# Kernel optimization log

Hardware: AMD Instinct MI355X
Metric: run time of the kernel (lower is better)

The kernel has to match this reference:

```python
import jax, jax.numpy as jnp
import numpy as np

LN_EPS = 1e-5


def setup_inputs() -> dict:
    N, E, D = 50000, 800000, 128
    H = 4 * D
    key = jax.random.key(0)
    ks = jax.random.split(key, 8)
    h = jax.random.normal(ks[0], (N, D), dtype=jnp.float32)
    e_ij = jax.random.normal(ks[1], (E, D), dtype=jnp.float32)
    src = jax.random.randint(ks[2], (E,), 0, N, dtype=jnp.int32)
    dst = jax.random.randint(ks[3], (E,), 0, N, dtype=jnp.int32)
    # MLP params (torch nn.Linear default-style scale)
    W1 = jax.random.normal(ks[4], (D, H), dtype=jnp.float32) / np.sqrt(D)
    b1 = jnp.zeros((H,), dtype=jnp.float32)
    W2 = jax.random.normal(ks[5], (H, D), dtype=jnp.float32) / np.sqrt(H)
    b2 = jnp.zeros((D,), dtype=jnp.float32)
    gamma = jnp.ones((D,), dtype=jnp.float32)
    beta = jnp.zeros((D,), dtype=jnp.float32)
    return {"h": h, "e_ij": e_ij, "src": src, "dst": dst,
            "W1": W1, "b1": b1, "W2": W2, "b2": b2,
            "gamma": gamma, "beta": beta}


def reference(h, e_ij, src, dst, W1, b1, W2, b2, gamma, beta):
    N = h.shape[0]
    # update_all(copy_u('h'), sum): sum source-node features at each destination
    neigh = jax.ops.segment_sum(h[src], dst, num_segments=N)
    # update_all(copy_edge('e_ij'), sum): sum edge features at each destination
    u_edge = jax.ops.segment_sum(e_ij, dst, num_segments=N)
    u = neigh + u_edge                      # [N, D]
    # MLP: D -> 4D -> D with ReLU, then residual
    hid = jax.nn.relu(u @ W1 + b1)          # [N, 4D]
    out = hid @ W2 + b2 + h                 # [N, D]
    # LayerNorm over feature dim
    mean = jnp.mean(out, axis=-1, keepdims=True)
    var = jnp.var(out, axis=-1, keepdims=True)
    normed = (out - mean) * jax.lax.rsqrt(var + LN_EPS)
    # dropout with training=False is identity
    return normed * gamma + beta
```

## Files before the change

### kernel.cpp

```cpp
#include <hip/hip_runtime.h>

#define BM 64

typedef __bf16 bf16x8 __attribute__((ext_vector_type(8)));
typedef float f32x4 __attribute__((ext_vector_type(4)));
typedef float f4 __attribute__((ext_vector_type(4)));

__device__ __forceinline__ unsigned short f2bf(float x) {
  unsigned int u = __builtin_bit_cast(unsigned int, x);
  u += 0x7fffu + ((u >> 16) & 1u);
  return (unsigned short)(u >> 16);
}

__device__ __forceinline__ int swz(int row, int col) {
  return (row * 128 + col) ^ ((row & 7) << 3);
}

__device__ __forceinline__ f4 ntload4(const float* p) {
  return __builtin_nontemporal_load((const f4*)p);
}

__device__ __forceinline__ int wave_incl_scan(int v, int lane) {
  #pragma unroll
  for (int off = 1; off < 64; off <<= 1) {
    int t = __shfl_up(v, off, 64);
    if (lane >= off) v += t;
  }
  return v;
}

__global__ __launch_bounds__(256) void prep_weights(
    const float* __restrict__ W1, const float* __restrict__ W2,
    unsigned short* __restrict__ W1T, unsigned short* __restrict__ W2T,
    int* __restrict__ counts, int N) {
  int t = blockIdx.x * 256 + threadIdx.x;
  if (t < N) counts[t] = 0;
  {
    int hh = t >> 7, kk = t & 127;
    W1T[t] = f2bf(W1[kk * 512 + hh]);
  }
  {
    int dd = t >> 9, hh = t & 511;
    W2T[t] = f2bf(W2[hh * 128 + dd]);
  }
}

__global__ __launch_bounds__(256) void hist_dst(const int* __restrict__ dst,
                                                int* counts, int E) {
  int i = blockIdx.x * 256 + threadIdx.x;
  if (i < E) atomicAdd(&counts[dst[i]], 1);
}

__global__ __launch_bounds__(256) void scan1(const int* __restrict__ counts,
                                             int* offs, int* btot, int N) {
  int i = blockIdx.x * 256 + threadIdx.x;
  int lane = threadIdx.x & 63, wv = threadIdx.x >> 6;
  int v = (i < N) ? counts[i] : 0;
  int incl = wave_incl_scan(v, lane);
  __shared__ int wt[4];
  if (lane == 63) wt[wv] = incl;
  __syncthreads();
  int wpre = 0;
  for (int w = 0; w < wv; ++w) wpre += wt[w];
  if (i < N) offs[i] = wpre + incl - v;
  if (threadIdx.x == 255) btot[blockIdx.x] = wpre + incl;
}

__global__ __launch_bounds__(64) void scan2(int* btot, int nb) {
  int lane = threadIdx.x;
  __shared__ int carry_s;
  if (lane == 0) carry_s = 0;
  __syncthreads();
  for (int base = 0; base < nb; base += 64) {
    int i = base + lane;
    int v = (i < nb) ? btot[i] : 0;
    int incl = wave_incl_scan(v, lane);
    int carry = carry_s;
    if (i < nb) btot[i] = carry + incl - v;
    __syncthreads();
    if (lane == 63) carry_s = carry + incl;
    __syncthreads();
  }
}

__global__ __launch_bounds__(256) void scan3(int* offs, const int* __restrict__ btot,
                                             int N) {
  int i = blockIdx.x * 256 + threadIdx.x;
  if (i < N) offs[i] += btot[blockIdx.x];
}

__global__ __launch_bounds__(256) void build_perm(const int* __restrict__ dst,
                                                  const int* __restrict__ src,
                                                  int* offs, int2* perm2, int E) {
  int i = blockIdx.x * 256 + threadIdx.x;
  if (i < E) {
    int p = atomicAdd(&offs[dst[i]], 1);
    perm2[p] = make_int2(i, src[i]);
  }
}

__global__ __launch_bounds__(256) void gather_sum(
    const float* __restrict__ hfeat, const float* __restrict__ eij,
    const int2* __restrict__ perm2,
    const int* __restrict__ offs, const int* __restrict__ counts,
    float* __restrict__ u, int N) {
  int node = blockIdx.x * 4 + (threadIdx.x >> 6);
  if (node >= N) return;
  int lane = threadIdx.x & 63;
  int half = lane >> 5, c4 = (lane & 31) * 4;
  int cnt = counts[node];
  int beg = offs[node] - cnt;
  f4 acc = (f4){0.f, 0.f, 0.f, 0.f};
  for (int base = 0; base < cnt; base += 64) {
    int m = cnt - base; if (m > 64) m = 64;
    int2 es = perm2[beg + base + (lane < m ? lane : m - 1)];
    int k = 0;
    for (; 2 * k + 8 <= m; k += 4) {
      int i0 = 2 * k + half;
      int e0 = __shfl(es.x, i0, 64),     s0 = __shfl(es.y, i0, 64);
      int e1 = __shfl(es.x, i0 + 2, 64), s1 = __shfl(es.y, i0 + 2, 64);
      int e2 = __shfl(es.x, i0 + 4, 64), s2 = __shfl(es.y, i0 + 4, 64);
      int e3 = __shfl(es.x, i0 + 6, 64), s3 = __shfl(es.y, i0 + 6, 64);
      f4 ev0 = ntload4(eij + (size_t)e0 * 128 + c4);
      f4 ev1 = ntload4(eij + (size_t)e1 * 128 + c4);
      f4 ev2 = ntload4(eij + (size_t)e2 * 128 + c4);
      f4 ev3 = ntload4(eij + (size_t)e3 * 128 + c4);
      f4 hv0 = *(const f4*)(hfeat + (size_t)s0 * 128 + c4);
      f4 hv1 = *(const f4*)(hfeat + (size_t)s1 * 128 + c4);
      f4 hv2 = *(const f4*)(hfeat + (size_t)s2 * 128 + c4);
      f4 hv3 = *(const f4*)(hfeat + (size_t)s3 * 128 + c4);
      acc += (ev0 + hv0) + (ev1 + hv1) + (ev2 + hv2) + (ev3 + hv3);
    }
    for (; 2 * k < m; ++k) {
      int idx = 2 * k + half;
      int e = __shfl(es.x, idx & 63, 64), s = __shfl(es.y, idx & 63, 64);
      if (idx < m) {
        f4 ev = ntload4(eij + (size_t)e * 128 + c4);
        f4 hv = *(const f4*)(hfeat + (size_t)s * 128 + c4);
        acc += ev + hv;
      }
    }
  }
  acc.x += __shfl_xor(acc.x, 32, 64);
  acc.y += __shfl_xor(acc.y, 32, 64);
  acc.z += __shfl_xor(acc.z, 32, 64);
  acc.w += __shfl_xor(acc.w, 32, 64);
  if (half == 0) *(f4*)(u + (size_t)node * 128 + c4) = acc;
}

__global__ __launch_bounds__(256, 2) void fused_mlp_ln(
    float* uo, const float* __restrict__ hfeat,
    const unsigned short* __restrict__ W1T, const unsigned short* __restrict__ W2T,
    const float* __restrict__ b1, const float* __restrict__ b2,
    const float* __restrict__ gma, const float* __restrict__ bta, int N) {
  __shared__ unsigned short As[BM * 128];
  __shared__ unsigned short Hs[BM * 128];
  __shared__ unsigned short Bs[128 * 128];

  const int tid = threadIdx.x;
  const int wave = tid >> 6, lane = tid & 63;
  const int lo = lane & 15, hi = lane >> 4;
  const int bm0 = blockIdx.x * BM;
  const int arow = wave * 16 + lo;

  #pragma unroll
  for (int i = 0; i < 8; ++i) {
    int q = i * 256 + tid;
    int r = q >> 5, c4 = (q & 31) * 4;
    f4 v = (f4){0.f, 0.f, 0.f, 0.f};
    if (bm0 + r < N) v = *(const f4*)(uo + (size_t)(bm0 + r) * 128 + c4);
    uint2 bv;
    bv.x = (unsigned)f2bf(v.x) | ((unsigned)f2bf(v.y) << 16);
    bv.y = (unsigned)f2bf(v.z) | ((unsigned)f2bf(v.w) << 16);
    *(uint2*)(&As[swz(r, c4)]) = bv;
  }

  f32x4 acc2[8];
  #pragma unroll
  for (int n = 0; n < 8; ++n) acc2[n] = (f32x4){0.f, 0.f, 0.f, 0.f};

  for (int c = 0; c < 4; ++c) {
    __syncthreads();
    #pragma unroll
    for (int i = 0; i < 8; ++i) {
      int q = i * 256 + tid;
      int r = q >> 4, c8 = (q & 15) * 8;
      uint4 w = *(const uint4*)(W1T + ((size_t)(c * 128 + r) * 128 + c8));
      *(uint4*)(&Bs[swz(r, c8)]) = w;
    }
    __syncthreads();

    f32x4 acc1[8];
    #pragma unroll
    for (int n = 0; n < 8; ++n) acc1[n] = (f32x4){0.f, 0.f, 0.f, 0.f};
    #pragma unroll
    for (int kk = 0; kk < 4; ++kk) {
      bf16x8 a = *(const bf16x8*)(&As[swz(arow, kk * 32 + hi * 8)]);
      #pragma unroll
      for (int n = 0; n < 8; ++n) {
        bf16x8 b = *(const bf16x8*)(&Bs[swz(n * 16 + lo, kk * 32 + hi * 8)]);
        acc1[n] = __builtin_amdgcn_mfma_f32_16x16x32_bf16(a, b, acc1[n], 0, 0, 0);
      }
    }
    #pragma unroll
    for (int n = 0; n < 8; ++n) {
      float bb = b1[c * 128 + n * 16 + lo];
      #pragma unroll
      for (int j = 0; j < 4; ++j) {
        float v = acc1[n][j] + bb;
        v = v > 0.f ? v : 0.f;
        Hs[swz(wave * 16 + hi * 4 + j, n * 16 + lo)] = f2bf(v);
      }
    }
    __syncthreads();
    #pragma unroll
    for (int i = 0; i < 8; ++i) {
      int q = i * 256 + tid;
      int r = q >> 4, c8 = (q & 15) * 8;
      uint4 w = *(const uint4*)(W2T + ((size_t)r * 512 + c * 128 + c8));
      *(uint4*)(&Bs[swz(r, c8)]) = w;
    }
    __syncthreads();
    #pragma unroll
    for (int kk = 0; kk < 4; ++kk) {
      bf16x8 a = *(const bf16x8*)(&Hs[swz(arow, kk * 32 + hi * 8)]);
      #pragma unroll
      for (int n = 0; n < 8; ++n) {
        bf16x8 b = *(const bf16x8*)(&Bs[swz(n * 16 + lo, kk * 32 + hi * 8)]);
        acc2[n] = __builtin_amdgcn_mfma_f32_16x16x32_bf16(a, b, acc2[n], 0, 0, 0);
      }
    }
  }

  float b2v[8], gv[8], bv2[8];
  #pragma unroll
  for (int n = 0; n < 8; ++n) {
    int d = n * 16 + lo;
    b2v[n] = b2[d]; gv[n] = gma[d]; bv2[n] = bta[d];
  }
  #pragma unroll
  for (int j = 0; j < 4; ++j) {
    int m = wave * 16 + hi * 4 + j;
    int grow = bm0 + m;
    bool valid = grow < N;
    float vals[8];
    float s = 0.f, s2 = 0.f;
    #pragma unroll
    for (int n = 0; n < 8; ++n) {
      float hres = valid ? hfeat[(size_t)grow * 128 + n * 16 + lo] : 0.f;
      float v = acc2[n][j] + b2v[n] + hres;
      vals[n] = v;
      s += v; s2 += v * v;
    }
    #pragma unroll
    for (int mk = 1; mk < 16; mk <<= 1) {
      s  += __shfl_xor(s, mk, 64);
      s2 += __shfl_xor(s2, mk, 64);
    }
    float mean = s * (1.f / 128.f);
    float var = s2 * (1.f / 128.f) - mean * mean;
    float inv = rsqrtf(var + 1e-5f);
    if (valid) {
      #pragma unroll
      for (int n = 0; n < 8; ++n) {
        uo[(size_t)grow * 128 + n * 16 + lo] = (vals[n] - mean) * inv * gv[n] + bv2[n];
      }
    }
  }
}

extern "C" void kernel_launch(void* const* d_in, const int* in_sizes, int n_in,
                              void* d_out, int out_size, void* d_ws, size_t ws_size,
                              hipStream_t stream) {
  (void)n_in; (void)out_size; (void)ws_size;
  const float* hfeat = (const float*)d_in[0];
  const float* eij   = (const float*)d_in[1];
  const int*   src   = (const int*)d_in[2];
  const int*   dst   = (const int*)d_in[3];
  const float* W1    = (const float*)d_in[4];
  const float* b1    = (const float*)d_in[5];
  const float* W2    = (const float*)d_in[6];
  const float* b2    = (const float*)d_in[7];
  const float* gma   = (const float*)d_in[8];
  const float* bta   = (const float*)d_in[9];
  float* out = (float*)d_out;

  int N = in_sizes[0] / 128;
  int E = in_sizes[2];
  int nb1 = (N + 255) / 256;

  char* ws = (char*)d_ws;
  unsigned short* W1T = (unsigned short*)ws;              ws += 512 * 128 * 2;
  unsigned short* W2T = (unsigned short*)ws;              ws += 128 * 512 * 2;
  int* counts = (int*)ws;                                 ws += (size_t)N * 4;
  int* offs   = (int*)ws;                                 ws += (size_t)N * 4;
  int* btot   = (int*)ws;                                 ws += ((nb1 + 63) / 64) * 64 * 4;
  ws = (char*)(((uintptr_t)ws + 255) & ~(uintptr_t)255);
  int2* perm2 = (int2*)ws;                                ws += (size_t)E * 8;

  prep_weights<<<256, 256, 0, stream>>>(W1, W2, W1T, W2T, counts, N);
  hist_dst<<<(E + 255) / 256, 256, 0, stream>>>(dst, counts, E);
  scan1<<<nb1, 256, 0, stream>>>(counts, offs, btot, N);
  scan2<<<1, 64, 0, stream>>>(btot, nb1);
  scan3<<<nb1, 256, 0, stream>>>(offs, btot, N);
  build_perm<<<(E + 255) / 256, 256, 0, stream>>>(dst, src, offs, perm2, E);

  gather_sum<<<(N + 3) / 4, 256, 0, stream>>>(hfeat, eij, perm2, offs, counts,
                                              out, N);

  fused_mlp_ln<<<(N + BM - 1) / BM, 256, 0, stream>>>(out, hfeat, W1T, W2T,
                                                      b1, b2, gma, bta, N);
}
```

Before: 264.5 us.

## Fuse gather-sum aggregation into the MLP+LayerNorm kernel prologue

Moves the per-node neighbour/edge gather-sum into the fused MLP kernel. Each wave now aggregates 16 rows in sequence and writes them straight into the bf16 shared-memory A tile, so the fp32 intermediate no longer goes to global memory and back, and one launch is removed. In exchange, gather parallelism drops: the grid now has N/64 blocks with launch_bounds(256,2) instead of N/4 blocks. Gather latency is also serialized with the MFMA work inside each block rather than overlapped across many independent blocks.

```diff
diff --git a/kernel.cpp b/kernel.cpp
--- a/kernel.cpp
+++ b/kernel.cpp
@@ -99,60 +99,14 @@
   }
 }
 
-__global__ __launch_bounds__(256) void gather_sum(
+__global__ __launch_bounds__(256, 2) void fused_gather_mlp_ln(
     const float* __restrict__ hfeat, const float* __restrict__ eij,
     const int2* __restrict__ perm2,
     const int* __restrict__ offs, const int* __restrict__ counts,
-    float* __restrict__ u, int N) {
-  int node = blockIdx.x * 4 + (threadIdx.x >> 6);
-  if (node >= N) return;
-  int lane = threadIdx.x & 63;
-  int half = lane >> 5, c4 = (lane & 31) * 4;
-  int cnt = counts[node];
-  int beg = offs[node] - cnt;
-  f4 acc = (f4){0.f, 0.f, 0.f, 0.f};
-  for (int base = 0; base < cnt; base += 64) {
-    int m = cnt - base; if (m > 64) m = 64;
-    int2 es = perm2[beg + base + (lane < m ? lane : m - 1)];
-    int k = 0;
-    for (; 2 * k + 8 <= m; k += 4) {
-      int i0 = 2 * k + half;
-      int e0 = __shfl(es.x, i0, 64),     s0 = __shfl(es.y, i0, 64);
-      int e1 = __shfl(es.x, i0 + 2, 64), s1 = __shfl(es.y, i0 + 2, 64);
-      int e2 = __shfl(es.x, i0 + 4, 64), s2 = __shfl(es.y, i0 + 4, 64);
-      int e3 = __shfl(es.x, i0 + 6, 64), s3 = __shfl(es.y, i0 + 6, 64);
-      f4 ev0 = ntload4(eij + (size_t)e0 * 128 + c4);
-      f4 ev1 = ntload4(eij + (size_t)e1 * 128 + c4);
-      f4 ev2 = ntload4(eij + (size_t)e2 * 128 + c4);
-      f4 ev3 = ntload4(eij + (size_t)e3 * 128 + c4);
-      f4 hv0 = *(const f4*)(hfeat + (size_t)s0 * 128 + c4);
-      f4 hv1 = *(const f4*)(hfeat + (size_t)s1 * 128 + c4);
-      f4 hv2 = *(const f4*)(hfeat + (size_t)s2 * 128 + c4);
-      f4 hv3 = *(const f4*)(hfeat + (size_t)s3 * 128 + c4);
-      acc += (ev0 + hv0) + (ev1 + hv1) + (ev2 + hv2) + (ev3 + hv3);
-    }
-    for (; 2 * k < m; ++k) {
-      int idx = 2 * k + half;
-      int e = __shfl(es.x, idx & 63, 64), s = __shfl(es.y, idx & 63, 64);
-      if (idx < m) {
-        f4 ev = ntload4(eij + (size_t)e * 128 + c4);
-        f4 hv = *(const f4*)(hfeat + (size_t)s * 128 + c4);
-        acc += ev + hv;
-      }
-    }
-  }
-  acc.x += __shfl_xor(acc.x, 32, 64);
-  acc.y += __shfl_xor(acc.y, 32, 64);
-  acc.z += __shfl_xor(acc.z, 32, 64);
-  acc.w += __shfl_xor(acc.w, 32, 64);
-  if (half == 0) *(f4*)(u + (size_t)node * 128 + c4) = acc;
-}
-
-__global__ __launch_bounds__(256, 2) void fused_mlp_ln(
-    float* uo, const float* __restrict__ hfeat,
     const unsigned short* __restrict__ W1T, const unsigned short* __restrict__ W2T,
     const float* __restrict__ b1, const float* __restrict__ b2,
-    const float* __restrict__ gma, const float* __restrict__ bta, int N) {
+    const float* __restrict__ gma, const float* __restrict__ bta,
+    float* __restrict__ out, int N) {
   __shared__ unsigned short As[BM * 128];
   __shared__ unsigned short Hs[BM * 128];
   __shared__ unsigned short Bs[128 * 128];
@@ -162,17 +116,56 @@
   const int lo = lane & 15, hi = lane >> 4;
   const int bm0 = blockIdx.x * BM;
   const int arow = wave * 16 + lo;
-
-  #pragma unroll
-  for (int i = 0; i < 8; ++i) {
-    int q = i * 256 + tid;
-    int r = q >> 5, c4 = (q & 31) * 4;
-    f4 v = (f4){0.f, 0.f, 0.f, 0.f};
-    if (bm0 + r < N) v = *(const f4*)(uo + (size_t)(bm0 + r) * 128 + c4);
-    uint2 bv;
-    bv.x = (unsigned)f2bf(v.x) | ((unsigned)f2bf(v.y) << 16);
-    bv.y = (unsigned)f2bf(v.z) | ((unsigned)f2bf(v.w) << 16);
-    *(uint2*)(&As[swz(r, c4)]) = bv;
+  const int half = lane >> 5, c4 = (lane & 31) * 4;
+
+  for (int t = 0; t < 16; ++t) {
+    int r = wave * 16 + t;
+    int node = bm0 + r;
+    f4 acc = (f4){0.f, 0.f, 0.f, 0.f};
+    if (node < N) {
+      int cnt = counts[node];
+      int beg = offs[node] - cnt;
+      for (int base = 0; base < cnt; base += 64) {
+        int m = cnt - base; if (m > 64) m = 64;
+        int2 es = perm2[beg + base + (lane < m ? lane : m - 1)];
+        int k = 0;
+        for (; 2 * k + 8 <= m; k += 4) {
+          int i0 = 2 * k + half;
+          int e0 = __shfl(es.x, i0, 64),     s0 = __shfl(es.y, i0, 64);
+          int e1 = __shfl(es.x, i0 + 2, 64), s1 = __shfl(es.y, i0 + 2, 64);
+          int e2 = __shfl(es.x, i0 + 4, 64), s2 = __shfl(es.y, i0 + 4, 64);
+          int e3 = __shfl(es.x, i0 + 6, 64), s3 = __shfl(es.y, i0 + 6, 64);
+          f4 ev0 = ntload4(eij + (size_t)e0 * 128 + c4);
+          f4 ev1 = ntload4(eij + (size_t)e1 * 128 + c4);
+          f4 ev2 = ntload4(eij + (size_t)e2 * 128 + c4);
+          f4 ev3 = ntload4(eij + (size_t)e3 * 128 + c4);
+          f4 hv0 = *(const f4*)(hfeat + (size_t)s0 * 128 + c4);
+          f4 hv1 = *(const f4*)(hfeat + (size_t)s1 * 128 + c4);
+          f4 hv2 = *(const f4*)(hfeat + (size_t)s2 * 128 + c4);
+          f4 hv3 = *(const f4*)(hfeat + (size_t)s3 * 128 + c4);
+          acc += (ev0 + hv0) + (ev1 + hv1) + (ev2 + hv2) + (ev3 + hv3);
+        }
+        for (; 2 * k < m; ++k) {
+          int idx = 2 * k + half;
+          int e = __shfl(es.x, idx & 63, 64), s = __shfl(es.y, idx & 63, 64);
+          if (idx < m) {
+            f4 ev = ntload4(eij + (size_t)e * 128 + c4);
+            f4 hv = *(const f4*)(hfeat + (size_t)s * 128 + c4);
+            acc += ev + hv;
+          }
+        }
+      }
+    }
+    acc.x += __shfl_xor(acc.x, 32, 64);
+    acc.y += __shfl_xor(acc.y, 32, 64);
+    acc.z += __shfl_xor(acc.z, 32, 64);
+    acc.w += __shfl_xor(acc.w, 32, 64);
+    if (half == 0) {
+      uint2 bv;
+      bv.x = (unsigned)f2bf(acc.x) | ((unsigned)f2bf(acc.y) << 16);
+      bv.y = (unsigned)f2bf(acc.z) | ((unsigned)f2bf(acc.w) << 16);
+      *(uint2*)(&As[swz(r, c4)]) = bv;
+    }
   }
 
   f32x4 acc2[8];
@@ -263,7 +256,7 @@
     if (valid) {
       #pragma unroll
       for (int n = 0; n < 8; ++n) {
-        uo[(size_t)grow * 128 + n * 16 + lo] = (vals[n] - mean) * inv * gv[n] + bv2[n];
+        out[(size_t)grow * 128 + n * 16 + lo] = (vals[n] - mean) * inv * gv[n] + bv2[n];
       }
     }
   }
@@ -305,9 +298,6 @@
   scan3<<<nb1, 256, 0, stream>>>(offs, btot, N);
   build_perm<<<(E + 255) / 256, 256, 0, stream>>>(dst, src, offs, perm2, E);
 
-  gather_sum<<<(N + 3) / 4, 256, 0, stream>>>(hfeat, eij, perm2, offs, counts,
-                                              out, N);
-
-  fused_mlp_ln<<<(N + BM - 1) / BM, 256, 0, stream>>>(out, hfeat, W1T, W2T,
-                                                      b1, b2, gma, bta, N);
-}
+  fused_gather_mlp_ln<<<(N + BM - 1) / BM, 256, 0, stream>>>(
+      hfeat, eij, perm2, offs, counts, W1T, W2T, b1, b2, gma, bta, out, N);
+}
```

New measurement: 285.3 us. 1.08x slower.
